# Optimization experiments

Hardware: AMD Instinct MI355X
Metric: run time of the kernel (lower is better)

## Reference

```python
import jax, jax.numpy as jnp
import numpy as np

NUM_HEADS = 12
LN_EPS = 1e-12


def setup_inputs() -> dict:
    key = jax.random.key(0)
    ks = jax.random.split(key, 18)
    B, S, H, I, P, KW = 8, 128, 768, 3072, 50, 100
    s = 0.02
    inp = {
        'hidden_state': jax.random.normal(ks[0], (B, S, H), jnp.float32),
        'positive_keywords': jax.random.normal(ks[1], (P, H), jnp.float32),
        'negative_keywords': jax.random.normal(ks[2], (P, H), jnp.float32),
        'attention_mask': jnp.zeros((B, 1, 1, S), jnp.float32),
        # Bilinear weights: out = (x @ W) * keyword
        'Wq': jax.random.normal(ks[3], (H, H), jnp.float32) * s,
        'Wk': jax.random.normal(ks[4], (H, H), jnp.float32) * s,
        'Wv': jax.random.normal(ks[5], (H, H), jnp.float32) * s,
        'Wo': jax.random.normal(ks[6], (H, H), jnp.float32) * s,
        'bo': jnp.zeros((H,), jnp.float32),
        # mlp: Linear(kwcount, 1)
        'Wmlp': jax.random.normal(ks[7], (KW,), jnp.float32) * s,
        'bmlp': jnp.zeros((), jnp.float32),
        # Bottleneck FFN
        'Wdown': jax.random.normal(ks[8], (H, I), jnp.float32) * s,
        'bdown': jnp.zeros((I,), jnp.float32),
        'Wup': jax.random.normal(ks[9], (I, H), jnp.float32) * s,
        'bup': jnp.zeros((H,), jnp.float32),
        'gamma': jnp.ones((H,), jnp.float32),
        'beta': jnp.zeros((H,), jnp.float32),
    }
    return inp


def reference(hidden_state, positive_keywords, negative_keywords, attention_mask,
              Wq, Wk, Wv, Wo, bo, Wmlp, bmlp, Wdown, bdown, Wup, bup, gamma, beta):
    B, S, H = hidden_state.shape
    nh = NUM_HEADS
    hd = H // nh
    # interleave pos/neg keywords -> pool [KW, H] (diff == 0, no padding)
    pool = jnp.stack((positive_keywords, negative_keywords), axis=1).reshape(-1, H)

    # shared sequence projections (keyword modulates elementwise afterwards)
    PQ = hidden_state @ Wq  # [B,S,H]
    PK = hidden_state @ Wk
    PV = hidden_state @ Wv
    scale = 1.0 / jnp.sqrt(jnp.float32(hd))

    def per_kw(kw):  # kw: [H]
        def heads(P):
            return (P * kw).reshape(B, S, nh, hd).transpose(0, 2, 1, 3)  # [B,nh,S,hd]
        Q, K, V = heads(PQ), heads(PK), heads(PV)
        scores = jnp.einsum('bhqd,bhkd->bhqk', Q, K) * scale + attention_mask
        # NOTE: softmax over dim=-2 (query axis), faithful to the original
        w = jax.nn.softmax(scores, axis=-2)
        ctx = jnp.einsum('bhqk,bhkd->bhqd', w, V)
        ctx = ctx.transpose(0, 2, 1, 3).reshape(B, S, H)
        return ctx @ Wo + bo  # [B,S,H]

    stacked = jax.vmap(per_kw)(pool)  # [KW,B,S,H]
    # mlp Linear(KW,1) over the stacked keyword axis
    fused = jnp.einsum('kbsh,k->bsh', stacked, Wmlp) + bmlp  # [B,S,H]

    # Bottleneck FFN + residual LayerNorm (dropout = identity in eval)
    down = jax.nn.gelu(fused @ Wdown + bdown, approximate=False)
    up = down @ Wup + bup
    x = up + fused
    mu = jnp.mean(x, axis=-1, keepdims=True)
    var = jnp.var(x, axis=-1, keepdims=True)
    return gamma * (x - mu) / jnp.sqrt(var + LN_EPS) + beta
```

## Files before the change

kernel.cpp:

```cpp
#include <hip/hip_runtime.h>
#include <hip/hip_bf16.h>
#include <math.h>

#define B_ 8
#define S_ 128
#define H_ 768
#define NH_ 12
#define HD_ 64
#define M_ 1024
#define KW_ 100
#define I_ 3072
#define QKVN 2304
#define NCHUNK 5
#define KWPER 20
#define LOG2E 1.4426950408889634f

typedef __attribute__((ext_vector_type(8))) short short8;
typedef __attribute__((ext_vector_type(8))) unsigned short ushort8;
typedef __attribute__((ext_vector_type(4))) float f32x4;
typedef __attribute__((ext_vector_type(4))) short s4b;

static __device__ __forceinline__ unsigned short f2b(float f) {
  union { float f; unsigned int u; } v; v.f = f;
  return (unsigned short)((v.u + 0x7fffu + ((v.u >> 16) & 1u)) >> 16);
}
static __device__ __forceinline__ float b2f(unsigned short b) {
  union { unsigned int u; float f; } v; v.u = ((unsigned int)b) << 16;
  return v.f;
}

__global__ void k_prep(const float* __restrict__ hidden,
                       const float* __restrict__ Wq, const float* __restrict__ Wk,
                       const float* __restrict__ Wv, const float* __restrict__ Wo,
                       const float* __restrict__ Wdown, const float* __restrict__ Wup,
                       const float* __restrict__ posk, const float* __restrict__ negk,
                       const float* __restrict__ Wmlp, const float* __restrict__ bmlp,
                       const float* __restrict__ bo,
                       unsigned short* __restrict__ hb, unsigned short* __restrict__ qkvT,
                       unsigned short* __restrict__ WoT, unsigned short* __restrict__ WdownT,
                       unsigned short* __restrict__ WupT,
                       float* __restrict__ kw2s, float* __restrict__ kwm, float* __restrict__ c0) {
  __shared__ float tile[32][33];
  int z = blockIdx.z;
  int t = threadIdx.x;
  if (z == 6) {
    int n = blockIdx.y * 96 + blockIdx.x;
    if (n < 768) {
      int i = (n * 256 + t) * 4;
      float4 v = *(const float4*)&hidden[i];
      uint2 o;
      o.x = (unsigned)f2b(v.x) | ((unsigned)f2b(v.y) << 16);
      o.y = (unsigned)f2b(v.z) | ((unsigned)f2b(v.w) << 16);
      *(uint2*)&hb[i] = o;
    } else if (n < 1068) {
      int idx = (n - 768) * 256 + t;
      if (idx < KW_ * H_) {
        int j = idx / H_, d = idx - j * H_;
        float v = (j & 1) ? negk[(j >> 1) * H_ + d] : posk[(j >> 1) * H_ + d];
        kw2s[idx] = v * v * 0.125f * LOG2E;
        kwm[idx] = v * Wmlp[j];
      }
    } else if (n == 1068) {
      __shared__ float red[256];
      red[t] = (t < KW_) ? Wmlp[t] : 0.f;
      __syncthreads();
      for (int s = 128; s > 0; s >>= 1) { if (t < s) red[t] += red[t + s]; __syncthreads(); }
      float sWm = red[0];
      for (int c = t; c < H_; c += 256) c0[c] = sWm * bo[c] + bmlp[0];
    }
    return;
  }
  const float* src; unsigned short* dst; int R, C, r0, c0t;
  if (z < 4) {
    if (blockIdx.x >= 24) return;
    const float* srcs[4] = {Wq, Wk, Wv, Wo};
    src = srcs[z];
    dst = (z < 3) ? qkvT + (size_t)z * 768 * 768 : WoT;
    R = 768; C = 768; c0t = blockIdx.x * 32; r0 = blockIdx.y * 32;
  } else if (z == 4) {
    src = Wdown; dst = WdownT; R = 768; C = 3072;
    c0t = blockIdx.x * 32; r0 = blockIdx.y * 32;
  } else {
    src = Wup; dst = WupT; R = 3072; C = 768;
    c0t = blockIdx.y * 32; r0 = blockIdx.x * 32;
  }
  int tx = t & 31, ty = t >> 5;
#pragma unroll
  for (int i = 0; i < 4; i++)
    tile[ty + i * 8][tx] = src[(size_t)(r0 + ty + i * 8) * C + c0t + tx];
  __syncthreads();
#pragma unroll
  for (int i = 0; i < 4; i++)
    dst[(size_t)(c0t + ty + i * 8) * R + r0 + tx] = f2b(tile[tx][ty + i * 8]);
}

template <int EPI>
__launch_bounds__(256)
__global__ void k_gemm_bt(const unsigned short* __restrict__ A, const unsigned short* __restrict__ BT,
                          int M, int N, int K,
                          float* __restrict__ outF, unsigned short* __restrict__ outB,
                          const float* __restrict__ bias, const float* __restrict__ res) {
  __shared__ unsigned short Asm[128][56];
  __shared__ unsigned short Bsm[128][56];
  int tid = threadIdx.x;
  int lane = tid & 63, wid = tid >> 6;
  int g = lane >> 4, c16 = lane & 15;
  int wr = wid >> 1, wc = wid & 1;
  int m0 = blockIdx.y * 128, n0 = blockIdx.x * 128;
  f32x4 acc[4][4] = {};
  int r = tid >> 1, half = (tid & 1) * 16;
  const unsigned short* Ap = A + (size_t)(m0 + r) * K + half;
  const unsigned short* Bp = BT + (size_t)(n0 + r) * K + half;
  for (int kt = 0; kt < K; kt += 32) {
    __syncthreads();
    ushort8 a0 = *(const ushort8*)(Ap + kt);
    ushort8 a1 = *(const ushort8*)(Ap + kt + 8);
    ushort8 b0 = *(const ushort8*)(Bp + kt);
    ushort8 b1 = *(const ushort8*)(Bp + kt + 8);
    *(ushort8*)&Asm[r][half] = a0;  *(ushort8*)&Asm[r][half + 8] = a1;
    *(ushort8*)&Bsm[r][half] = b0;  *(ushort8*)&Bsm[r][half + 8] = b1;
    __syncthreads();
    short8 af[4], bf[4];
#pragma unroll
    for (int mi = 0; mi < 4; mi++) af[mi] = *(const short8*)&Asm[wr * 64 + mi * 16 + c16][g * 8];
#pragma unroll
    for (int ni = 0; ni < 4; ni++) bf[ni] = *(const short8*)&Bsm[wc * 64 + ni * 16 + c16][g * 8];
#pragma unroll
    for (int mi = 0; mi < 4; mi++)
#pragma unroll
      for (int ni = 0; ni < 4; ni++)
        acc[mi][ni] = __builtin_amdgcn_mfma_f32_16x16x32_bf16(af[mi], bf[ni], acc[mi][ni], 0, 0, 0);
  }
#pragma unroll
  for (int mi = 0; mi < 4; mi++)
#pragma unroll
    for (int ni = 0; ni < 4; ni++)
#pragma unroll
      for (int rr = 0; rr < 4; rr++) {
        int row = m0 + wr * 64 + mi * 16 + g * 4 + rr;
        int col = n0 + wc * 64 + ni * 16 + c16;
        float v = acc[mi][ni][rr];
        if (EPI == 0) {
          outB[(size_t)row * N + col] = f2b(v);
        } else if (EPI == 2) {
          float t = v + bias[col];
          float gl = 0.5f * t * (1.f + erff(t * 0.70710678118f));
          outB[(size_t)row * N + col] = f2b(gl);
        }
      }
}

__launch_bounds__(256)
__global__ void k_gemm_sk(const unsigned short* __restrict__ A, const unsigned short* __restrict__ BT,
                          int M, int N, int K, int ksl, float* __restrict__ pOut) {
  __shared__ unsigned short Asm[128][56];
  __shared__ unsigned short Bsm[128][56];
  int tid = threadIdx.x;
  int lane = tid & 63, wid = tid >> 6;
  int g = lane >> 4, c16 = lane & 15;
  int wr = wid >> 1, wc = wid & 1;
  int m0 = blockIdx.y * 128, n0 = blockIdx.x * 128;
  int kstart = blockIdx.z * ksl;
  f32x4 acc[4][4] = {};
  int r = tid >> 1, half = (tid & 1) * 16;
  const unsigned short* Ap = A + (size_t)(m0 + r) * K + half + kstart;
  const unsigned short* Bp = BT + (size_t)(n0 + r) * K + half + kstart;
  for (int kt = 0; kt < ksl; kt += 32) {
    __syncthreads();
    ushort8 a0 = *(const ushort8*)(Ap + kt);
    ushort8 a1 = *(const ushort8*)(Ap + kt + 8);
    ushort8 b0 = *(const ushort8*)(Bp + kt);
    ushort8 b1 = *(const ushort8*)(Bp + kt + 8);
    *(ushort8*)&Asm[r][half] = a0;  *(ushort8*)&Asm[r][half + 8] = a1;
    *(ushort8*)&Bsm[r][half] = b0;  *(ushort8*)&Bsm[r][half + 8] = b1;
    __syncthreads();
    short8 af[4], bf[4];
#pragma unroll
    for (int mi = 0; mi < 4; mi++) af[mi] = *(const short8*)&Asm[wr * 64 + mi * 16 + c16][g * 8];
#pragma unroll
    for (int ni = 0; ni < 4; ni++) bf[ni] = *(const short8*)&Bsm[wc * 64 + ni * 16 + c16][g * 8];
#pragma unroll
    for (int mi = 0; mi < 4; mi++)
#pragma unroll
      for (int ni = 0; ni < 4; ni++)
        acc[mi][ni] = __builtin_amdgcn_mfma_f32_16x16x32_bf16(af[mi], bf[ni], acc[mi][ni], 0, 0, 0);
  }
  float* dst = pOut + (size_t)blockIdx.z * M * N;
#pragma unroll
  for (int mi = 0; mi < 4; mi++)
#pragma unroll
    for (int ni = 0; ni < 4; ni++)
#pragma unroll
      for (int rr = 0; rr < 4; rr++) {
        int row = m0 + wr * 64 + mi * 16 + g * 4 + rr;
        int col = n0 + wc * 64 + ni * 16 + c16;
        dst[(size_t)row * N + col] = acc[mi][ni][rr];
      }
}

template <int SPLITS, int EPI>
__global__ void k_red(const float* __restrict__ p, const float* __restrict__ bias,
                      float* __restrict__ outF, unsigned short* __restrict__ outB, int N) {
  int i = (blockIdx.x * 256 + threadIdx.x) * 4;
  const size_t MN = (size_t)M_ * N;
  float4 s = *(const float4*)&p[i];
#pragma unroll
  for (int c = 1; c < SPLITS; c++) {
    float4 v = *(const float4*)&p[c * MN + i];
    s.x += v.x; s.y += v.y; s.z += v.z; s.w += v.w;
  }
  if (EPI == 1) {
    int col = i % N;
    s.x += bias[col]; s.y += bias[col + 1]; s.z += bias[col + 2]; s.w += bias[col + 3];
    *(float4*)&outF[i] = s;
  }
  uint2 o;
  o.x = (unsigned)f2b(s.x) | ((unsigned)f2b(s.y) << 16);
  o.y = (unsigned)f2b(s.z) | ((unsigned)f2b(s.w) << 16);
  *(uint2*)&outB[i] = o;
}

__launch_bounds__(512, 2)
__global__ void k_attn(const unsigned short* __restrict__ PQKV,
                       const float* __restrict__ kw2s, const float* __restrict__ kwm,
                       unsigned short* __restrict__ partial) {
  __shared__ __align__(16) char SM[67584];
  int tid = threadIdx.x;
  int lane = tid & 63, wid = tid >> 6;
  int g = (lane >> 4) & 3, c16 = lane & 15;
  int chunk = blockIdx.x, h = blockIdx.y, b = blockIdx.z;
  const size_t rowbase = (size_t)b * 128 * QKVN;
  const unsigned short* Qbase = PQKV + rowbase + h * HD_;
  const unsigned short* Kbase = Qbase + H_;
  const unsigned short* Vbase = Qbase + 2 * H_;

  unsigned short (*QS)[72] = (unsigned short(*)[72])SM;
  unsigned short (*VS)[72] = (unsigned short(*)[72])(SM + 18432);
  {
    int kq = tid >> 2, quarter = tid & 3;
    const unsigned short* srcq = Qbase + (size_t)kq * QKVN + quarter * 16;
    ushort8 a0 = *(const ushort8*)srcq;
    ushort8 a1 = *(const ushort8*)(srcq + 8);
    *(ushort8*)&QS[kq][quarter * 16] = a0;
    *(ushort8*)&QS[kq][quarter * 16 + 8] = a1;
    const unsigned short* srcv = Vbase + (size_t)kq * QKVN + quarter * 16;
    ushort8 w0 = *(const ushort8*)srcv;
    ushort8 w1 = *(const ushort8*)(srcv + 8);
    *(ushort8*)&VS[kq][quarter * 16] = w0;
    *(ushort8*)&VS[kq][quarter * 16 + 8] = w1;
  }
  const unsigned short* kpg = Kbase + (size_t)(wid * 16 + c16) * QKVN;
  ushort8 kraw0 = *(const ushort8*)(kpg + g * 8);
  ushort8 kraw1 = *(const ushort8*)(kpg + 32 + g * 8);
  __syncthreads();
  unsigned short vraw[4][4];
#pragma unroll
  for (int dt = 0; dt < 4; dt++)
#pragma unroll
    for (int j = 0; j < 4; j++)
      vraw[dt][j] = VS[wid * 16 + 4 * g + j][dt * 16 + c16];

  f32x4 acc[4][8] = {};
  int zo = 0;
  asm volatile("" : "+v"(zo));
  for (int ki = 0; ki < KWPER; ki++) {
    int kwi = chunk * KWPER + ki;
    const float* k2p = kw2s + (size_t)kwi * H_ + h * HD_;
    const float* kmp = kwm + (size_t)kwi * H_ + h * HD_;
    short8 kA0, kA1;
    {
      float4 s0 = *(const float4*)(k2p + g * 8);
      float4 s1 = *(const float4*)(k2p + g * 8 + 4);
      float4 s2 = *(const float4*)(k2p + 32 + g * 8);
      float4 s3 = *(const float4*)(k2p + 32 + g * 8 + 4);
      union { unsigned u[4]; short8 v; } p0, p1;
      asm("v_cvt_pk_bf16_f32 %0, %1, %2" : "=v"(p0.u[0]) : "v"(b2f(kraw0[0]) * s0.x), "v"(b2f(kraw0[1]) * s0.y));
      asm("v_cvt_pk_bf16_f32 %0, %1, %2" : "=v"(p0.u[1]) : "v"(b2f(kraw0[2]) * s0.z), "v"(b2f(kraw0[3]) * s0.w));
      asm("v_cvt_pk_bf16_f32 %0, %1, %2" : "=v"(p0.u[2]) : "v"(b2f(kraw0[4]) * s1.x), "v"(b2f(kraw0[5]) * s1.y));
      asm("v_cvt_pk_bf16_f32 %0, %1, %2" : "=v"(p0.u[3]) : "v"(b2f(kraw0[6]) * s1.z), "v"(b2f(kraw0[7]) * s1.w));
      asm("v_cvt_pk_bf16_f32 %0, %1, %2" : "=v"(p1.u[0]) : "v"(b2f(kraw1[0]) * s2.x), "v"(b2f(kraw1[1]) * s2.y));
      asm("v_cvt_pk_bf16_f32 %0, %1, %2" : "=v"(p1.u[1]) : "v"(b2f(kraw1[2]) * s2.z), "v"(b2f(kraw1[3]) * s2.w));
      asm("v_cvt_pk_bf16_f32 %0, %1, %2" : "=v"(p1.u[2]) : "v"(b2f(kraw1[4]) * s3.x), "v"(b2f(kraw1[5]) * s3.y));
      asm("v_cvt_pk_bf16_f32 %0, %1, %2" : "=v"(p1.u[3]) : "v"(b2f(kraw1[6]) * s3.z), "v"(b2f(kraw1[7]) * s3.w));
      kA0 = p0.v; kA1 = p1.v;
    }
    s4b vA[4];
#pragma unroll
    for (int dt = 0; dt < 4; dt++) {
      float km = kmp[dt * 16 + c16];
      union { unsigned u[2]; s4b v; } pv;
      asm("v_cvt_pk_bf16_f32 %0, %1, %2" : "=v"(pv.u[0]) : "v"(b2f(vraw[dt][0]) * km), "v"(b2f(vraw[dt][1]) * km));
      asm("v_cvt_pk_bf16_f32 %0, %1, %2" : "=v"(pv.u[1]) : "v"(b2f(vraw[dt][2]) * km), "v"(b2f(vraw[dt][3]) * km));
      vA[dt] = pv.v;
    }
    f32x4 sc[8];
    __builtin_amdgcn_s_setprio(1);
#pragma unroll
    for (int t = 0; t < 8; t++) {
      short8 q0 = *(const short8*)&QS[16 * t + c16][g * 8 + zo];
      short8 q1 = *(const short8*)&QS[16 * t + c16][32 + g * 8 + zo];
      f32x4 z = {0.f, 0.f, 0.f, 0.f};
      z = __builtin_amdgcn_mfma_f32_16x16x32_bf16(kA0, q0, z, 0, 0, 0);
      z = __builtin_amdgcn_mfma_f32_16x16x32_bf16(kA1, q1, z, 0, 0, 0);
      sc[t][0] = __builtin_amdgcn_exp2f(z[0]);
      sc[t][1] = __builtin_amdgcn_exp2f(z[1]);
      sc[t][2] = __builtin_amdgcn_exp2f(z[2]);
      sc[t][3] = __builtin_amdgcn_exp2f(z[3]);
    }
    __builtin_amdgcn_s_setprio(0);
    float cs[4];
#pragma unroll
    for (int rr = 0; rr < 4; rr++) {
      float s = sc[0][rr];
#pragma unroll
      for (int t = 1; t < 8; t++) s += sc[t][rr];
      s += __shfl_xor(s, 1);
      s += __shfl_xor(s, 2);
      s += __shfl_xor(s, 4);
      s += __shfl_xor(s, 8);
      cs[rr] = __builtin_amdgcn_rcpf(s);
    }
    s4b pw[8];
#pragma unroll
    for (int t = 0; t < 8; t++) {
      union { unsigned u[2]; s4b v; } pp;
      asm("v_cvt_pk_bf16_f32 %0, %1, %2" : "=v"(pp.u[0]) : "v"(sc[t][0] * cs[0]), "v"(sc[t][1] * cs[1]));
      asm("v_cvt_pk_bf16_f32 %0, %1, %2" : "=v"(pp.u[1]) : "v"(sc[t][2] * cs[2]), "v"(sc[t][3] * cs[3]));
      pw[t] = pp.v;
    }
    __builtin_amdgcn_s_setprio(1);
#pragma unroll
    for (int dt = 0; dt < 4; dt++)
#pragma unroll
      for (int t = 0; t < 8; t++)
        acc[dt][t] = __builtin_amdgcn_mfma_f32_16x16x16bf16_1k(vA[dt], pw[t], acc[dt][t], 0, 0, 0);
    __builtin_amdgcn_s_setprio(0);
  }
  float (*Ebuf)[16][132] = (float(*)[16][132])SM;
  int qo = tid & 127, db = (tid >> 7) * 4;
#pragma unroll
  for (int dt = 0; dt < 4; dt++) {
    __syncthreads();
#pragma unroll
    for (int t = 0; t < 8; t++)
#pragma unroll
      for (int rr = 0; rr < 4; rr++)
        Ebuf[wid][4 * g + rr][16 * t + c16] = acc[dt][t][rr];
    __syncthreads();
    float s0 = 0.f, s1 = 0.f, s2 = 0.f, s3 = 0.f;
#pragma unroll
    for (int w = 0; w < 8; w++) {
      s0 += Ebuf[w][db + 0][qo];
      s1 += Ebuf[w][db + 1][qo];
      s2 += Ebuf[w][db + 2][qo];
      s3 += Ebuf[w][db + 3][qo];
    }
    unsigned short* o = partial + (size_t)chunk * M_ * H_ + (size_t)(b * 128 + qo) * H_ + h * HD_ + dt * 16 + db;
    uint2 ov;
    ov.x = (unsigned)f2b(s0) | ((unsigned)f2b(s1) << 16);
    ov.y = (unsigned)f2b(s2) | ((unsigned)f2b(s3) << 16);
    *(uint2*)o = ov;
  }
}

__global__ void k_reduce(const unsigned short* __restrict__ partial, unsigned short* __restrict__ ctxsum) {
  int i = (blockIdx.x * 256 + threadIdx.x) * 4;
  float s0 = 0.f, s1 = 0.f, s2 = 0.f, s3 = 0.f;
#pragma unroll
  for (int c = 0; c < NCHUNK; c++) {
    uint2 v = *(const uint2*)&partial[(size_t)c * M_ * H_ + i];
    s0 += b2f((unsigned short)(v.x & 0xffffu));
    s1 += b2f((unsigned short)(v.x >> 16));
    s2 += b2f((unsigned short)(v.y & 0xffffu));
    s3 += b2f((unsigned short)(v.y >> 16));
  }
  uint2 o;
  o.x = (unsigned)f2b(s0) | ((unsigned)f2b(s1) << 16);
  o.y = (unsigned)f2b(s2) | ((unsigned)f2b(s3) << 16);
  *(uint2*)&ctxsum[i] = o;
}

__launch_bounds__(256)
__global__ void k_ln2(const float* __restrict__ pUp, const float* __restrict__ bup,
                      const float* __restrict__ fusedF,
                      const float* __restrict__ gamma, const float* __restrict__ beta,
                      float* __restrict__ out) {
  __shared__ float red[8];
  int row = blockIdx.x, t = threadIdx.x;
  int lane = t & 63, wid = t >> 6;
  const size_t MN = (size_t)M_ * H_;
  const size_t rb = (size_t)row * H_;
  float v[3];
#pragma unroll
  for (int j = 0; j < 3; j++) {
    int c = t + j * 256;
    float x = pUp[rb + c] + pUp[MN + rb + c] + pUp[2 * MN + rb + c] + pUp[3 * MN + rb + c];
    v[j] = x + bup[c] + fusedF[rb + c];
  }
  float s = v[0] + v[1] + v[2];
#pragma unroll
  for (int off = 1; off < 64; off <<= 1) s += __shfl_xor(s, off);
  if (lane == 0) red[wid] = s;
  __syncthreads();
  float mu = (red[0] + red[1] + red[2] + red[3]) * (1.f / 768.f);
  float q = 0.f;
#pragma unroll
  for (int j = 0; j < 3; j++) { float d = v[j] - mu; q += d * d; }
#pragma unroll
  for (int off = 1; off < 64; off <<= 1) q += __shfl_xor(q, off);
  if (lane == 0) red[4 + wid] = q;
  __syncthreads();
  float var = (red[4] + red[5] + red[6] + red[7]) * (1.f / 768.f);
  float rstd = rsqrtf(var + 1e-12f);
#pragma unroll
  for (int j = 0; j < 3; j++) {
    int c = t + j * 256;
    out[rb + c] = gamma[c] * ((v[j] - mu) * rstd) + beta[c];
  }
}


extern "C" void kernel_launch(void* const* d_in, const int* in_sizes, int n_in,
                              void* d_out, int out_size, void* d_ws, size_t ws_size,
                              hipStream_t stream) {
  const float* hidden = (const float*)d_in[0];
  const float* posk   = (const float*)d_in[1];
  const float* negk   = (const float*)d_in[2];
  const float* Wq     = (const float*)d_in[4];
  const float* Wk     = (const float*)d_in[5];
  const float* Wv     = (const float*)d_in[6];
  const float* Wo     = (const float*)d_in[7];
  const float* bo     = (const float*)d_in[8];
  const float* Wmlp   = (const float*)d_in[9];
  const float* bmlp   = (const float*)d_in[10];
  const float* Wdown  = (const float*)d_in[11];
  const float* bdown  = (const float*)d_in[12];
  const float* Wup    = (const float*)d_in[13];
  const float* bup    = (const float*)d_in[14];
  const float* gamma  = (const float*)d_in[15];
  const float* beta   = (const float*)d_in[16];

  char* ws = (char*)d_ws;
  size_t off = 0;
  auto alloc = [&](size_t bytes) -> void* {
    void* p = ws + off;
    off += (bytes + 255) & ~(size_t)255;
    return p;
  };
  unsigned short* hb     = (unsigned short*)alloc((size_t)M_ * H_ * 2);
  unsigned short* qkvT   = (unsigned short*)alloc((size_t)QKVN * H_ * 2);
  unsigned short* WoT    = (unsigned short*)alloc((size_t)H_ * H_ * 2);
  unsigned short* WdownT = (unsigned short*)alloc((size_t)I_ * H_ * 2);
  unsigned short* WupT   = (unsigned short*)alloc((size_t)H_ * I_ * 2);
  unsigned short* PQKV   = (unsigned short*)alloc((size_t)M_ * QKVN * 2);
  float* kw2s    = (float*)alloc((size_t)KW_ * H_ * 4);
  float* kwm     = (float*)alloc((size_t)KW_ * H_ * 4);
  float* c0      = (float*)alloc((size_t)H_ * 4);
  float* partial = (float*)alloc((size_t)10 * M_ * H_ * 4);
  unsigned short* ctxsum = (unsigned short*)alloc((size_t)M_ * H_ * 2);
  float* fusedF  = (float*)alloc((size_t)M_ * H_ * 4);
  unsigned short* fusedB = (unsigned short*)alloc((size_t)M_ * H_ * 2);
  unsigned short* downB  = (unsigned short*)alloc((size_t)M_ * I_ * 2);

  k_prep<<<dim3(96, 24, 7), 256, 0, stream>>>(hidden, Wq, Wk, Wv, Wo, Wdown, Wup,
                                              posk, negk, Wmlp, bmlp, bo,
                                              hb, qkvT, WoT, WdownT, WupT, kw2s, kwm, c0);
  k_gemm_sk<<<dim3(18, 8, 2), 256, 0, stream>>>(hb, qkvT, M_, QKVN, H_, 384, partial);
  k_red<2, 0><<<2304, 256, 0, stream>>>(partial, nullptr, nullptr, PQKV, QKVN);
  k_attn<<<dim3(NCHUNK, NH_, B_), 512, 0, stream>>>(PQKV, kw2s, kwm, (unsigned short*)partial);
  k_reduce<<<768, 256, 0, stream>>>((const unsigned short*)partial, ctxsum);
  k_gemm_sk<<<dim3(6, 8, 4), 256, 0, stream>>>(ctxsum, WoT, M_, H_, H_, 192, partial);
  k_red<4, 1><<<768, 256, 0, stream>>>(partial, c0, fusedF, fusedB, H_);
  k_gemm_bt<2><<<dim3(24, 8), 256, 0, stream>>>(fusedB, WdownT, M_, I_, H_, nullptr, downB, bdown, nullptr);
  k_gemm_sk<<<dim3(6, 8, 4), 256, 0, stream>>>(downB, WupT, M_, H_, I_, 768, partial);
  k_ln2<<<M_, 256, 0, stream>>>(partial, bup, fusedF, gamma, beta, (float*)d_out);
}
```

Before: 179.7 us.

## Use direct global-to-LDS loads in GEMMs and stage keyword scales in LDS

Both GEMM kernels now load the A and B tiles with global_load_lds (16 bytes per lane) straight into an unpadded 128x32 LDS layout. This skips the register round trip and the explicit LDS stores. The attention kernel also preloads its chunk's keyword scale vectors into shared memory once, so the inner keyword loop no longer reads them from global memory. The unpadded GEMM layout may cause LDS bank conflicts on the fragment reads, and the extra 10 KB of LDS in the attention kernel may reduce occupancy.

```diff
diff --git a/kernel.cpp b/kernel.cpp
--- a/kernel.cpp
+++ b/kernel.cpp
@@ -27,6 +27,10 @@
 static __device__ __forceinline__ float b2f(unsigned short b) {
   union { unsigned int u; float f; } v; v.u = ((unsigned int)b) << 16;
   return v.f;
+}
+static __device__ __forceinline__ void gload16(const unsigned short* g, unsigned short* l) {
+  __builtin_amdgcn_global_load_lds((const __attribute__((address_space(1))) unsigned int*)g,
+                                   (__attribute__((address_space(3))) unsigned int*)l, 16, 0, 0);
 }
 
 __global__ void k_prep(const float* __restrict__ hidden,
@@ -100,31 +104,29 @@
                           int M, int N, int K,
                           float* __restrict__ outF, unsigned short* __restrict__ outB,
                           const float* __restrict__ bias, const float* __restrict__ res) {
-  __shared__ unsigned short Asm[128][56];
-  __shared__ unsigned short Bsm[128][56];
+  __shared__ __align__(16) unsigned short Asm[128 * 32];
+  __shared__ __align__(16) unsigned short Bsm[128 * 32];
   int tid = threadIdx.x;
   int lane = tid & 63, wid = tid >> 6;
   int g = lane >> 4, c16 = lane & 15;
   int wr = wid >> 1, wc = wid & 1;
   int m0 = blockIdx.y * 128, n0 = blockIdx.x * 128;
   f32x4 acc[4][4] = {};
-  int r = tid >> 1, half = (tid & 1) * 16;
-  const unsigned short* Ap = A + (size_t)(m0 + r) * K + half;
-  const unsigned short* Bp = BT + (size_t)(n0 + r) * K + half;
+  int ldsrow = lane >> 2, ldscol = (lane & 3) * 8;
   for (int kt = 0; kt < K; kt += 32) {
     __syncthreads();
-    ushort8 a0 = *(const ushort8*)(Ap + kt);
-    ushort8 a1 = *(const ushort8*)(Ap + kt + 8);
-    ushort8 b0 = *(const ushort8*)(Bp + kt);
-    ushort8 b1 = *(const ushort8*)(Bp + kt + 8);
-    *(ushort8*)&Asm[r][half] = a0;  *(ushort8*)&Asm[r][half + 8] = a1;
-    *(ushort8*)&Bsm[r][half] = b0;  *(ushort8*)&Bsm[r][half + 8] = b1;
+#pragma unroll
+    for (int r = 0; r < 2; r++) {
+      int c = wid * 2 + r;
+      gload16(A + (size_t)(m0 + c * 16 + ldsrow) * K + kt + ldscol, &Asm[c * 512 + lane * 8]);
+      gload16(BT + (size_t)(n0 + c * 16 + ldsrow) * K + kt + ldscol, &Bsm[c * 512 + lane * 8]);
+    }
     __syncthreads();
     short8 af[4], bf[4];
 #pragma unroll
-    for (int mi = 0; mi < 4; mi++) af[mi] = *(const short8*)&Asm[wr * 64 + mi * 16 + c16][g * 8];
-#pragma unroll
-    for (int ni = 0; ni < 4; ni++) bf[ni] = *(const short8*)&Bsm[wc * 64 + ni * 16 + c16][g * 8];
+    for (int mi = 0; mi < 4; mi++) af[mi] = *(const short8*)&Asm[(wr * 64 + mi * 16 + c16) * 32 + g * 8];
+#pragma unroll
+    for (int ni = 0; ni < 4; ni++) bf[ni] = *(const short8*)&Bsm[(wc * 64 + ni * 16 + c16) * 32 + g * 8];
 #pragma unroll
     for (int mi = 0; mi < 4; mi++)
 #pragma unroll
@@ -153,8 +155,8 @@
 __launch_bounds__(256)
 __global__ void k_gemm_sk(const unsigned short* __restrict__ A, const unsigned short* __restrict__ BT,
                           int M, int N, int K, int ksl, float* __restrict__ pOut) {
-  __shared__ unsigned short Asm[128][56];
-  __shared__ unsigned short Bsm[128][56];
+  __shared__ __align__(16) unsigned short Asm[128 * 32];
+  __shared__ __align__(16) unsigned short Bsm[128 * 32];
   int tid = threadIdx.x;
   int lane = tid & 63, wid = tid >> 6;
   int g = lane >> 4, c16 = lane & 15;
@@ -162,23 +164,21 @@
   int m0 = blockIdx.y * 128, n0 = blockIdx.x * 128;
   int kstart = blockIdx.z * ksl;
   f32x4 acc[4][4] = {};
-  int r = tid >> 1, half = (tid & 1) * 16;
-  const unsigned short* Ap = A + (size_t)(m0 + r) * K + half + kstart;
-  const unsigned short* Bp = BT + (size_t)(n0 + r) * K + half + kstart;
+  int ldsrow = lane >> 2, ldscol = (lane & 3) * 8;
   for (int kt = 0; kt < ksl; kt += 32) {
     __syncthreads();
-    ushort8 a0 = *(const ushort8*)(Ap + kt);
-    ushort8 a1 = *(const ushort8*)(Ap + kt + 8);
-    ushort8 b0 = *(const ushort8*)(Bp + kt);
-    ushort8 b1 = *(const ushort8*)(Bp + kt + 8);
-    *(ushort8*)&Asm[r][half] = a0;  *(ushort8*)&Asm[r][half + 8] = a1;
-    *(ushort8*)&Bsm[r][half] = b0;  *(ushort8*)&Bsm[r][half + 8] = b1;
+#pragma unroll
+    for (int r = 0; r < 2; r++) {
+      int c = wid * 2 + r;
+      gload16(A + (size_t)(m0 + c * 16 + ldsrow) * K + kstart + kt + ldscol, &Asm[c * 512 + lane * 8]);
+      gload16(BT + (size_t)(n0 + c * 16 + ldsrow) * K + kstart + kt + ldscol, &Bsm[c * 512 + lane * 8]);
+    }
     __syncthreads();
     short8 af[4], bf[4];
 #pragma unroll
-    for (int mi = 0; mi < 4; mi++) af[mi] = *(const short8*)&Asm[wr * 64 + mi * 16 + c16][g * 8];
-#pragma unroll
-    for (int ni = 0; ni < 4; ni++) bf[ni] = *(const short8*)&Bsm[wc * 64 + ni * 16 + c16][g * 8];
+    for (int mi = 0; mi < 4; mi++) af[mi] = *(const short8*)&Asm[(wr * 64 + mi * 16 + c16) * 32 + g * 8];
+#pragma unroll
+    for (int ni = 0; ni < 4; ni++) bf[ni] = *(const short8*)&Bsm[(wc * 64 + ni * 16 + c16) * 32 + g * 8];
 #pragma unroll
     for (int mi = 0; mi < 4; mi++)
 #pragma unroll
@@ -225,6 +225,8 @@
                        const float* __restrict__ kw2s, const float* __restrict__ kwm,
                        unsigned short* __restrict__ partial) {
   __shared__ __align__(16) char SM[67584];
+  __shared__ float kw2L[KWPER * 64];
+  __shared__ float kwmL[KWPER * 64];
   int tid = threadIdx.x;
   int lane = tid & 63, wid = tid >> 6;
   int g = (lane >> 4) & 3, c16 = lane & 15;
@@ -248,6 +250,12 @@
     ushort8 w1 = *(const ushort8*)(srcv + 8);
     *(ushort8*)&VS[kq][quarter * 16] = w0;
     *(ushort8*)&VS[kq][quarter * 16 + 8] = w1;
+    for (int i = tid; i < KWPER * 64; i += 512) {
+      int ki = i >> 6, d = i & 63;
+      size_t gi = (size_t)(chunk * KWPER + ki) * H_ + h * HD_ + d;
+      kw2L[i] = kw2s[gi];
+      kwmL[i] = kwm[gi];
+    }
   }
   const unsigned short* kpg = Kbase + (size_t)(wid * 16 + c16) * QKVN;
   ushort8 kraw0 = *(const ushort8*)(kpg + g * 8);
@@ -264,9 +272,8 @@
   int zo = 0;
   asm volatile("" : "+v"(zo));
   for (int ki = 0; ki < KWPER; ki++) {
-    int kwi = chunk * KWPER + ki;
-    const float* k2p = kw2s + (size_t)kwi * H_ + h * HD_;
-    const float* kmp = kwm + (size_t)kwi * H_ + h * HD_;
+    const float* k2p = &kw2L[ki * 64];
+    const float* kmp = &kwmL[ki * 64];
     short8 kA0, kA1;
     {
       float4 s0 = *(const float4*)(k2p + g * 8);
```

Measured after the change: 177.1 us. Within noise of the previous version (-1.4%).
